# Kernel tuning notes

Measured on AMD Instinct MI355X. Metric: run time of the kernel, lower is better.

The kernel has to match this reference:

```python
import jax, jax.numpy as jnp
import numpy as np

WINDOW_SIZE = 11
SIGMA = 1.5
C1 = 0.01 ** 2
C2 = 0.03 ** 2


def _gaussian_window(window_size=WINDOW_SIZE, sigma=SIGMA):
    coords = jnp.arange(window_size, dtype=jnp.float32) - window_size // 2
    g = jnp.exp(-(coords ** 2) / (2.0 * sigma ** 2))
    g = g / g.sum()
    w3d = g[:, None, None] * g[None, :, None] * g[None, None, :]
    w3d = w3d / w3d.sum()
    return w3d[None, None]  # [1, 1, K, K, K] (OIDHW)


def _gconv3d(x, window):
    # depthwise 3D conv, SAME padding (pad = K//2), groups = C
    C = x.shape[1]
    w = jnp.broadcast_to(window, (C, 1) + window.shape[2:])
    pad = window.shape[-1] // 2
    return jax.lax.conv_general_dilated(
        x, w,
        window_strides=(1, 1, 1),
        padding=[(pad, pad)] * 3,
        dimension_numbers=("NCDHW", "OIDHW", "NCDHW"),
        feature_group_count=C,
    )


def setup_inputs() -> dict:
    key = jax.random.key(0)
    k1, k2 = jax.random.split(key)
    shape = (4, 1, 64, 192, 192)  # [B, C, D, H, W]
    pred = jax.random.uniform(k1, shape, dtype=jnp.float32)
    target = jax.random.uniform(k2, shape, dtype=jnp.float32)
    return {"pred": pred, "target": target}


def reference(pred, target):
    window = _gaussian_window()
    mu_p = _gconv3d(pred, window)
    mu_t = _gconv3d(target, window)
    mu_p_sq = mu_p ** 2
    mu_t_sq = mu_t ** 2
    mu_pt = mu_p * mu_t
    sigma_p_sq = _gconv3d(pred ** 2, window) - mu_p_sq
    sigma_t_sq = _gconv3d(target ** 2, window) - mu_t_sq
    sigma_pt = _gconv3d(pred * target, window) - mu_pt
    ssim_map = ((2.0 * mu_pt + C1) * (2.0 * sigma_pt + C2)) / (
        (mu_p_sq + mu_t_sq + C1) * (sigma_p_sq + sigma_t_sq + C2)
    )
    return 1.0 - ssim_map.mean()
```

## Files before the change

kernel.cpp:

```cpp
#include <hip/hip_runtime.h>


#define D_DIM 64
#define H_DIM 192
#define W_DIM 192
#define SLICE (H_DIM * W_DIM)
#define VOL   (D_DIM * SLICE)
#define NB    4
#define KS    11
#define RAD   5
#define TH    32
#define TW    48
#define HT    (TH + 2 * RAD)
#define WTT   (TW + 2 * RAD)
#define SPITCH 59
#define IP2   48
#define IPF2  (HT * IP2)
#define C1F   (0.01f * 0.01f)
#define C2F   (0.03f * 0.03f)

typedef _Float16 h4 __attribute__((ext_vector_type(4)));

__device__ __forceinline__ void make_window(float* g) {
    float s = 0.f;
#pragma unroll
    for (int i = 0; i < KS; ++i) {
        float c = (float)(i - RAD);
        g[i] = expf(-(c * c) * (1.0f / 4.5f));
        s += g[i];
    }
    float inv = 1.0f / s;
#pragma unroll
    for (int i = 0; i < KS; ++i) g[i] *= inv;
}

__global__ __launch_bounds__(256) void hw_blur_kernel(
    const float* __restrict__ pred, const float* __restrict__ targ,
    uint2* __restrict__ Xg, unsigned short* __restrict__ Yg, int b0) {
    __shared__ union U {
        float stage[2 * HT * SPITCH];
        unsigned short obuf[5 * TH * TW];
    } u;
    __shared__ _Float16 interm2[5 * IPF2];
    float* sp = u.stage;
    float* st = u.stage + HT * SPITCH;

    float g[KS];
    make_window(g);

    const int tid = threadIdx.x;
    const int d    = blockIdx.y;
    const int tile = blockIdx.x;
    const int h0 = (tile >> 2) * TH;
    const int w0 = (tile & 3) * TW;
    const int bl = blockIdx.z;

    const int in_base = (b0 + bl) * VOL + d * SLICE;

    for (int i = tid; i < HT * SPITCH; i += 256) {
        int y = i / SPITCH, x = i - y * SPITCH;
        int gh = h0 + y - RAD, gw = w0 + x - RAD;
        float pv = 0.f, tv = 0.f;
        if (x < WTT && (unsigned)gh < (unsigned)H_DIM && (unsigned)gw < (unsigned)W_DIM) {
            int idx = in_base + gh * W_DIM + gw;
            pv = pred[idx];
            tv = targ[idx];
        }
        sp[i] = pv;
        st[i] = tv;
    }
    __syncthreads();

    if (tid < 252) {
        const int y = tid / 6;
        const int x0 = (tid % 6) * 8;
        float wp[18], wt[18];
#pragma unroll
        for (int k = 0; k < 18; ++k) {
            wp[k] = sp[y * SPITCH + x0 + k];
            wt[k] = st[y * SPITCH + x0 + k];
        }
#pragma unroll
        for (int o = 0; o < 8; ++o) {
            float s0 = 0.f, s1 = 0.f, s2 = 0.f, s3 = 0.f, s4 = 0.f;
#pragma unroll
            for (int k = 0; k < KS; ++k) {
                float pv = wp[o + k], tv = wt[o + k], gk = g[k];
                s0 += gk * pv;
                s1 += gk * tv;
                s2 += gk * pv * pv;
                s3 += gk * tv * tv;
                s4 += gk * pv * tv;
            }
            int idx = y * IP2 + x0 + o;
            interm2[0 * IPF2 + idx] = (_Float16)s0;
            interm2[1 * IPF2 + idx] = (_Float16)s1;
            interm2[2 * IPF2 + idx] = (_Float16)s2;
            interm2[3 * IPF2 + idx] = (_Float16)s3;
            interm2[4 * IPF2 + idx] = (_Float16)s4;
        }
    }
    __syncthreads();

    if (tid < 240) {
        const int f = tid / TW;
        const int x = tid % TW;
        const _Float16* col = interm2 + f * IPF2 + x;
        unsigned short* ob = u.obuf + f * (TH * TW) + x;
        float acc[KS];
#pragma unroll
        for (int s = 0; s < KS; ++s) acc[s] = 0.f;
#pragma unroll
        for (int yy = 0; yy < HT; ++yy) {
            float v = (float)col[yy * IP2];
#pragma unroll
            for (int m = 0; m < KS; ++m) {
                if (yy < 10 && m < 10 - yy) continue;
                acc[(yy + m + 1) % KS] += g[10 - m] * v;
            }
            if (yy >= 10) {
                const int y = yy - 10;
                const int s = (yy + 1) % KS;
                _Float16 h = (_Float16)acc[s];
                ob[y * TW] = *(unsigned short*)&h;
                acc[s] = 0.f;
            }
        }
    }
    __syncthreads();

    const size_t pl_base = (size_t)(bl * D_DIM + d) * SLICE;
#pragma unroll
    for (int it = 0; it < 6; ++it) {
        int px = it * 256 + tid;
        int y = px / TW, x = px - y * TW;
        unsigned a0 = u.obuf[0 * (TH * TW) + px];
        unsigned a1 = u.obuf[1 * (TH * TW) + px];
        unsigned a2 = u.obuf[2 * (TH * TW) + px];
        unsigned a3 = u.obuf[3 * (TH * TW) + px];
        unsigned a4 = u.obuf[4 * (TH * TW) + px];
        size_t gi = pl_base + (size_t)(h0 + y) * W_DIM + (w0 + x);
        Xg[gi] = make_uint2(a0 | (a1 << 16), a2 | (a3 << 16));
        Yg[gi] = (unsigned short)a4;
    }
}


#define LOADP(s, q) do {                                                  \
    const int _o = (q) * SLICE;                                           \
    h4 _v = x4[_o];                                                       \
    w0[s] = (float)_v[0]; w1[s] = (float)_v[1];                           \
    w2[s] = (float)_v[2]; w3[s] = (float)_v[3];                           \
    w4[s] = (float)y1[_o];                                                \
} while (0)

#define SSIM_ACC(MP, MT, E2, T2, PT) do {                                 \
    float _mps = (MP) * (MP), _mts = (MT) * (MT), _mpt = (MP) * (MT);     \
    float _num = (2.f * _mpt + C1F) * (2.f * ((PT) - _mpt) + C2F);        \
    float _den = (_mps + _mts + C1F) *                                    \
                 (((E2) - _mps) + ((T2) - _mts) + C2F);                   \
    ssim_sum += _num * __builtin_amdgcn_rcpf(_den);                       \
} while (0)

#define EMIT_W(r, JHI) do {                                               \
    float _mp = 0.f, _mt = 0.f, _e2 = 0.f, _t2 = 0.f, _pt = 0.f;          \
    _Pragma("unroll")                                                     \
    for (int _j = 0; _j <= (JHI); ++_j) {                                 \
        const int _s = (1 + (r) + _j) % 11; const float _g = g[_j];       \
        _mp += _g * w0[_s]; _mt += _g * w1[_s]; _e2 += _g * w2[_s];       \
        _t2 += _g * w3[_s]; _pt += _g * w4[_s];                           \
    }                                                                     \
    SSIM_ACC(_mp, _mt, _e2, _t2, _pt);                                    \
} while (0)

#define EMIT_IN(d) do {                                                   \
    float _mp = 0.f, _mt = 0.f, _e2 = 0.f, _t2 = 0.f, _pt = 0.f;          \
    _Pragma("unroll")                                                     \
    for (int _j = 5 - (d); _j < 11; ++_j) {                               \
        const int _s = (d) - 5 + _j; const float _g = g[_j];              \
        _mp += _g * w0[_s]; _mt += _g * w1[_s]; _e2 += _g * w2[_s];       \
        _t2 += _g * w3[_s]; _pt += _g * w4[_s];                           \
    }                                                                     \
    SSIM_ACC(_mp, _mt, _e2, _t2, _pt);                                    \
} while (0)

#define STEP(r, q) do { LOADP(r, q); EMIT_W(r, 10); } while (0)

__global__ __launch_bounds__(256) void dblur_ssim_kernel(
    const h4* __restrict__ Xg, const _Float16* __restrict__ Yg,
    float* __restrict__ partials) {
    float g[KS];
    make_window(g);

    const int tid = threadIdx.x;
    const int bl = blockIdx.x / 144;
    const int hw = (blockIdx.x % 144) * 256 + tid;
    const int cb = bl * VOL + hw;
    const h4* x4 = Xg + cb;
    const _Float16* y1 = Yg + cb;

    float w0[KS], w1[KS], w2[KS], w3[KS], w4[KS];
    float ssim_sum = 0.f;

    if (blockIdx.y == 0) {
        LOADP(0, 0); LOADP(1, 1); LOADP(2, 2); LOADP(3, 3); LOADP(4, 4);
        LOADP(5, 5); LOADP(6, 6); LOADP(7, 7); LOADP(8, 8); LOADP(9, 9);
        LOADP(10, 10);
        EMIT_IN(0); EMIT_IN(1); EMIT_IN(2); EMIT_IN(3); EMIT_IN(4); EMIT_IN(5);
#pragma unroll 1
        for (int b = 0; b < 2; ++b) {
            const int qb = 11 + 11 * b;
            STEP(0, qb + 0); STEP(1, qb + 1); STEP(2, qb + 2); STEP(3, qb + 3);
            STEP(4, qb + 4); STEP(5, qb + 5); STEP(6, qb + 6); STEP(7, qb + 7);
            STEP(8, qb + 8); STEP(9, qb + 9); STEP(10, qb + 10);
        }
        STEP(0, 33); STEP(1, 34); STEP(2, 35); STEP(3, 36);
    } else {
        LOADP(5, 27); LOADP(6, 28); LOADP(7, 29); LOADP(8, 30); LOADP(9, 31);
        LOADP(10, 32); LOADP(0, 33); LOADP(1, 34); LOADP(2, 35); LOADP(3, 36);
        LOADP(4, 37);
        EMIT_W(4, 10);
        STEP(5, 38); STEP(6, 39); STEP(7, 40); STEP(8, 41); STEP(9, 42);
        STEP(10, 43);
        {
            const int qb = 44;
            STEP(0, qb + 0); STEP(1, qb + 1); STEP(2, qb + 2); STEP(3, qb + 3);
            STEP(4, qb + 4); STEP(5, qb + 5); STEP(6, qb + 6); STEP(7, qb + 7);
            STEP(8, qb + 8); STEP(9, qb + 9); STEP(10, qb + 10);
        }
        STEP(0, 55); STEP(1, 56); STEP(2, 57); STEP(3, 58); STEP(4, 59);
        STEP(5, 60); STEP(6, 61); STEP(7, 62); STEP(8, 63);
        EMIT_W(9, 9); EMIT_W(10, 8); EMIT_W(11, 7); EMIT_W(12, 6); EMIT_W(13, 5);
    }

    float a = ssim_sum;
#pragma unroll
    for (int off = 32; off > 0; off >>= 1) a += __shfl_down(a, off, 64);
    __shared__ float red[4];
    int lane = tid & 63, wv = tid >> 6;
    if (lane == 0) red[wv] = a;
    __syncthreads();
    if (tid == 0)
        partials[blockIdx.y * gridDim.x + blockIdx.x] =
            red[0] + red[1] + red[2] + red[3];
}

__global__ __launch_bounds__(256) void finalize_kernel(
    const float* __restrict__ partials, int n, float* __restrict__ out) {
    double a = 0.0;
    for (int i = threadIdx.x; i < n; i += 256) a += (double)partials[i];
#pragma unroll
    for (int off = 32; off > 0; off >>= 1) a += __shfl_down(a, off, 64);
    __shared__ double red[4];
    int lane = threadIdx.x & 63, wv = threadIdx.x >> 6;
    if (lane == 0) red[wv] = a;
    __syncthreads();
    if (threadIdx.x == 0) {
        double s = red[0] + red[1] + red[2] + red[3];
        out[0] = (float)(1.0 - s / (double)((long long)NB * VOL));
    }
}

extern "C" void kernel_launch(void* const* d_in, const int* in_sizes, int n_in,
                              void* d_out, int out_size, void* d_ws, size_t ws_size,
                              hipStream_t stream) {
    const float* pred = (const float*)d_in[0];
    const float* targ = (const float*)d_in[1];
    float* out = (float*)d_out;

    int G = 4;
    while (G > 1 && (size_t)G * VOL * 10 + 8192 > ws_size) G >>= 1;

    uint2* Xg = (uint2*)d_ws;
    unsigned short* Yg = (unsigned short*)((char*)d_ws + (size_t)G * VOL * 8);
    float* partials = (float*)((char*)d_ws + (size_t)G * VOL * 10);
    const int bpc = G * 144;
    const int nchunks = NB / G;

    for (int c = 0; c < nchunks; ++c) {
        hw_blur_kernel<<<dim3(24, D_DIM, G), 256, 0, stream>>>(
            pred, targ, Xg, Yg, c * G);
        dblur_ssim_kernel<<<dim3(bpc, 2), 256, 0, stream>>>(
            (const h4*)Xg, (const _Float16*)Yg, partials + c * 2 * bpc);
    }
    finalize_kernel<<<1, 256, 0, stream>>>(partials, NB * 288, out);
}
```

Baseline: 216.5 us.

## Process two pixels per thread with packed half2 shared and wider global accesses

The HW blur kernel now stores intermediates as packed half2 words, so each vertical-pass thread handles two adjacent columns over half the rows, and the output is written as 16-byte X and 4-byte Y vectors. The depth-blur SSIM kernel now has each thread process two horizontally adjacent pixels using 16-byte and 4-byte loads, which halves the number of blocks. The aim is fewer, wider memory transactions and fewer LDS accesses, at the cost of doubled register arrays (ten 11-element windows), which may lower occupancy or cause spills.

```diff
diff --git a/kernel.cpp b/kernel.cpp
--- a/kernel.cpp
+++ b/kernel.cpp
@@ -14,12 +14,13 @@
 #define HT    (TH + 2 * RAD)
 #define WTT   (TW + 2 * RAD)
 #define SPITCH 59
-#define IP2   48
-#define IPF2  (HT * IP2)
+#define IP32  25
+#define IPF32 (HT * IP32)
 #define C1F   (0.01f * 0.01f)
 #define C2F   (0.03f * 0.03f)
 
-typedef _Float16 h4 __attribute__((ext_vector_type(4)));
+typedef _Float16 h2v __attribute__((ext_vector_type(2)));
+typedef _Float16 h8v __attribute__((ext_vector_type(8)));
 
 __device__ __forceinline__ void make_window(float* g) {
     float s = 0.f;
@@ -32,6 +33,12 @@
     float inv = 1.0f / s;
 #pragma unroll
     for (int i = 0; i < KS; ++i) g[i] *= inv;
+}
+
+__device__ __forceinline__ unsigned pk(float a, float b) {
+    unsigned lo = __builtin_bit_cast(unsigned short, (_Float16)a);
+    unsigned hi = __builtin_bit_cast(unsigned short, (_Float16)b);
+    return lo | (hi << 16);
 }
 
 __global__ __launch_bounds__(256) void hw_blur_kernel(
@@ -39,9 +46,9 @@
     uint2* __restrict__ Xg, unsigned short* __restrict__ Yg, int b0) {
     __shared__ union U {
         float stage[2 * HT * SPITCH];
-        unsigned short obuf[5 * TH * TW];
+        unsigned obuf32[5 * TH * (TW / 2)];
     } u;
-    __shared__ _Float16 interm2[5 * IPF2];
+    __shared__ unsigned interm32[5 * IPF32];
     float* sp = u.stage;
     float* st = u.stage + HT * SPITCH;
 
@@ -80,50 +87,59 @@
             wp[k] = sp[y * SPITCH + x0 + k];
             wt[k] = st[y * SPITCH + x0 + k];
         }
-#pragma unroll
-        for (int o = 0; o < 8; ++o) {
-            float s0 = 0.f, s1 = 0.f, s2 = 0.f, s3 = 0.f, s4 = 0.f;
-#pragma unroll
-            for (int k = 0; k < KS; ++k) {
-                float pv = wp[o + k], tv = wt[o + k], gk = g[k];
-                s0 += gk * pv;
-                s1 += gk * tv;
-                s2 += gk * pv * pv;
-                s3 += gk * tv * tv;
-                s4 += gk * pv * tv;
+        const int ib = y * IP32 + (x0 >> 1);
+#pragma unroll
+        for (int o = 0; o < 8; o += 2) {
+            float r0[2], r1[2], r2[2], r3[2], r4[2];
+#pragma unroll
+            for (int c = 0; c < 2; ++c) {
+                float s0 = 0.f, s1 = 0.f, s2 = 0.f, s3 = 0.f, s4 = 0.f;
+#pragma unroll
+                for (int k = 0; k < KS; ++k) {
+                    float pv = wp[o + c + k], tv = wt[o + c + k], gk = g[k];
+                    s0 += gk * pv;
+                    s1 += gk * tv;
+                    s2 += gk * pv * pv;
+                    s3 += gk * tv * tv;
+                    s4 += gk * pv * tv;
+                }
+                r0[c] = s0; r1[c] = s1; r2[c] = s2; r3[c] = s3; r4[c] = s4;
             }
-            int idx = y * IP2 + x0 + o;
-            interm2[0 * IPF2 + idx] = (_Float16)s0;
-            interm2[1 * IPF2 + idx] = (_Float16)s1;
-            interm2[2 * IPF2 + idx] = (_Float16)s2;
-            interm2[3 * IPF2 + idx] = (_Float16)s3;
-            interm2[4 * IPF2 + idx] = (_Float16)s4;
+            int idx = ib + (o >> 1);
+            interm32[0 * IPF32 + idx] = pk(r0[0], r0[1]);
+            interm32[1 * IPF32 + idx] = pk(r1[0], r1[1]);
+            interm32[2 * IPF32 + idx] = pk(r2[0], r2[1]);
+            interm32[3 * IPF32 + idx] = pk(r3[0], r3[1]);
+            interm32[4 * IPF32 + idx] = pk(r4[0], r4[1]);
         }
     }
     __syncthreads();
 
     if (tid < 240) {
-        const int f = tid / TW;
-        const int x = tid % TW;
-        const _Float16* col = interm2 + f * IPF2 + x;
-        unsigned short* ob = u.obuf + f * (TH * TW) + x;
-        float acc[KS];
-#pragma unroll
-        for (int s = 0; s < KS; ++s) acc[s] = 0.f;
-#pragma unroll
-        for (int yy = 0; yy < HT; ++yy) {
-            float v = (float)col[yy * IP2];
+        const int f  = tid / 48;
+        const int r  = tid % 48;
+        const int hh = r / 24;
+        const int p  = r % 24;
+        const unsigned* col = interm32 + f * IPF32 + (hh * 16) * IP32 + p;
+        unsigned* ob = u.obuf32 + f * (TH * (TW / 2)) + (hh * 16) * (TW / 2) + p;
+        float acc0[KS], acc1[KS];
+#pragma unroll
+        for (int s = 0; s < KS; ++s) { acc0[s] = 0.f; acc1[s] = 0.f; }
+#pragma unroll
+        for (int yy = 0; yy < 26; ++yy) {
+            h2v hv = __builtin_bit_cast(h2v, col[yy * IP32]);
+            float v0 = (float)hv[0], v1 = (float)hv[1];
 #pragma unroll
             for (int m = 0; m < KS; ++m) {
                 if (yy < 10 && m < 10 - yy) continue;
-                acc[(yy + m + 1) % KS] += g[10 - m] * v;
+                const int s = (yy + m + 1) % KS;
+                acc0[s] += g[10 - m] * v0;
+                acc1[s] += g[10 - m] * v1;
             }
             if (yy >= 10) {
-                const int y = yy - 10;
                 const int s = (yy + 1) % KS;
-                _Float16 h = (_Float16)acc[s];
-                ob[y * TW] = *(unsigned short*)&h;
-                acc[s] = 0.f;
+                ob[(yy - 10) * (TW / 2)] = pk(acc0[s], acc1[s]);
+                acc0[s] = 0.f; acc1[s] = 0.f;
             }
         }
     }
@@ -131,27 +147,33 @@
 
     const size_t pl_base = (size_t)(bl * D_DIM + d) * SLICE;
 #pragma unroll
-    for (int it = 0; it < 6; ++it) {
-        int px = it * 256 + tid;
-        int y = px / TW, x = px - y * TW;
-        unsigned a0 = u.obuf[0 * (TH * TW) + px];
-        unsigned a1 = u.obuf[1 * (TH * TW) + px];
-        unsigned a2 = u.obuf[2 * (TH * TW) + px];
-        unsigned a3 = u.obuf[3 * (TH * TW) + px];
-        unsigned a4 = u.obuf[4 * (TH * TW) + px];
-        size_t gi = pl_base + (size_t)(h0 + y) * W_DIM + (w0 + x);
-        Xg[gi] = make_uint2(a0 | (a1 << 16), a2 | (a3 << 16));
-        Yg[gi] = (unsigned short)a4;
+    for (int it = 0; it < 3; ++it) {
+        int pr = it * 256 + tid;
+        int y = pr / 24, xp = pr % 24;
+        unsigned a0 = u.obuf32[0 * 768 + pr];
+        unsigned a1 = u.obuf32[1 * 768 + pr];
+        unsigned a2 = u.obuf32[2 * 768 + pr];
+        unsigned a3 = u.obuf32[3 * 768 + pr];
+        unsigned a4 = u.obuf32[4 * 768 + pr];
+        size_t gi = pl_base + (size_t)(h0 + y) * W_DIM + (w0 + 2 * xp);
+        uint4 xv = make_uint4((a0 & 0xffffu) | (a1 << 16),
+                              (a2 & 0xffffu) | (a3 << 16),
+                              (a0 >> 16) | (a1 & 0xffff0000u),
+                              (a2 >> 16) | (a3 & 0xffff0000u));
+        *(uint4*)(Xg + gi) = xv;
+        *(unsigned*)(Yg + gi) = a4;
     }
 }
 
 
 #define LOADP(s, q) do {                                                  \
-    const int _o = (q) * SLICE;                                           \
-    h4 _v = x4[_o];                                                       \
-    w0[s] = (float)_v[0]; w1[s] = (float)_v[1];                           \
-    w2[s] = (float)_v[2]; w3[s] = (float)_v[3];                           \
-    w4[s] = (float)y1[_o];                                                \
+    h8v _v = x8[(q) * (SLICE / 2)];                                       \
+    h2v _y = __builtin_bit_cast(h2v, y2[(q) * (SLICE / 2)]);              \
+    wa0[s] = (float)_v[0]; wa1[s] = (float)_v[1];                         \
+    wa2[s] = (float)_v[2]; wa3[s] = (float)_v[3];                         \
+    wb0[s] = (float)_v[4]; wb1[s] = (float)_v[5];                         \
+    wb2[s] = (float)_v[6]; wb3[s] = (float)_v[7];                         \
+    wa4[s] = (float)_y[0]; wb4[s] = (float)_y[1];                         \
 } while (0)
 
 #define SSIM_ACC(MP, MT, E2, T2, PT) do {                                 \
@@ -163,43 +185,52 @@
 } while (0)
 
 #define EMIT_W(r, JHI) do {                                               \
-    float _mp = 0.f, _mt = 0.f, _e2 = 0.f, _t2 = 0.f, _pt = 0.f;          \
+    float _ap = 0.f, _at = 0.f, _a2 = 0.f, _a3 = 0.f, _a4 = 0.f;          \
+    float _bp = 0.f, _bt = 0.f, _b2 = 0.f, _b3 = 0.f, _b4 = 0.f;          \
     _Pragma("unroll")                                                     \
     for (int _j = 0; _j <= (JHI); ++_j) {                                 \
         const int _s = (1 + (r) + _j) % 11; const float _g = g[_j];       \
-        _mp += _g * w0[_s]; _mt += _g * w1[_s]; _e2 += _g * w2[_s];       \
-        _t2 += _g * w3[_s]; _pt += _g * w4[_s];                           \
+        _ap += _g * wa0[_s]; _at += _g * wa1[_s]; _a2 += _g * wa2[_s];    \
+        _a3 += _g * wa3[_s]; _a4 += _g * wa4[_s];                         \
+        _bp += _g * wb0[_s]; _bt += _g * wb1[_s]; _b2 += _g * wb2[_s];    \
+        _b3 += _g * wb3[_s]; _b4 += _g * wb4[_s];                         \
     }                                                                     \
-    SSIM_ACC(_mp, _mt, _e2, _t2, _pt);                                    \
+    SSIM_ACC(_ap, _at, _a2, _a3, _a4);                                    \
+    SSIM_ACC(_bp, _bt, _b2, _b3, _b4);                                    \
 } while (0)
 
 #define EMIT_IN(d) do {                                                   \
-    float _mp = 0.f, _mt = 0.f, _e2 = 0.f, _t2 = 0.f, _pt = 0.f;          \
+    float _ap = 0.f, _at = 0.f, _a2 = 0.f, _a3 = 0.f, _a4 = 0.f;          \
+    float _bp = 0.f, _bt = 0.f, _b2 = 0.f, _b3 = 0.f, _b4 = 0.f;          \
     _Pragma("unroll")                                                     \
     for (int _j = 5 - (d); _j < 11; ++_j) {                               \
         const int _s = (d) - 5 + _j; const float _g = g[_j];              \
-        _mp += _g * w0[_s]; _mt += _g * w1[_s]; _e2 += _g * w2[_s];       \
-        _t2 += _g * w3[_s]; _pt += _g * w4[_s];                           \
+        _ap += _g * wa0[_s]; _at += _g * wa1[_s]; _a2 += _g * wa2[_s];    \
+        _a3 += _g * wa3[_s]; _a4 += _g * wa4[_s];                         \
+        _bp += _g * wb0[_s]; _bt += _g * wb1[_s]; _b2 += _g * wb2[_s];    \
+        _b3 += _g * wb3[_s]; _b4 += _g * wb4[_s];                         \
     }                                                                     \
-    SSIM_ACC(_mp, _mt, _e2, _t2, _pt);                                    \
+    SSIM_ACC(_ap, _at, _a2, _a3, _a4);                                    \
+    SSIM_ACC(_bp, _bt, _b2, _b3, _b4);                                    \
 } while (0)
 
 #define STEP(r, q) do { LOADP(r, q); EMIT_W(r, 10); } while (0)
 
 __global__ __launch_bounds__(256) void dblur_ssim_kernel(
-    const h4* __restrict__ Xg, const _Float16* __restrict__ Yg,
+    const uint2* __restrict__ Xg, const unsigned short* __restrict__ Yg,
     float* __restrict__ partials) {
     float g[KS];
     make_window(g);
 
     const int tid = threadIdx.x;
-    const int bl = blockIdx.x / 144;
-    const int hw = (blockIdx.x % 144) * 256 + tid;
-    const int cb = bl * VOL + hw;
-    const h4* x4 = Xg + cb;
-    const _Float16* y1 = Yg + cb;
-
-    float w0[KS], w1[KS], w2[KS], w3[KS], w4[KS];
+    const int bl = blockIdx.x / 72;
+    const int hw0 = (blockIdx.x % 72) * 512 + tid * 2;
+    const int cb = bl * VOL + hw0;
+    const h8v* x8 = (const h8v*)Xg + (cb >> 1);
+    const unsigned* y2 = (const unsigned*)Yg + (cb >> 1);
+
+    float wa0[KS], wa1[KS], wa2[KS], wa3[KS], wa4[KS];
+    float wb0[KS], wb1[KS], wb2[KS], wb3[KS], wb4[KS];
     float ssim_sum = 0.f;
 
     if (blockIdx.y == 0) {
@@ -222,7 +253,8 @@
         EMIT_W(4, 10);
         STEP(5, 38); STEP(6, 39); STEP(7, 40); STEP(8, 41); STEP(9, 42);
         STEP(10, 43);
-        {
+#pragma unroll 1
+        for (int b = 0; b < 1; ++b) {
             const int qb = 44;
             STEP(0, qb + 0); STEP(1, qb + 1); STEP(2, qb + 2); STEP(3, qb + 3);
             STEP(4, qb + 4); STEP(5, qb + 5); STEP(6, qb + 6); STEP(7, qb + 7);
@@ -274,14 +306,14 @@
     uint2* Xg = (uint2*)d_ws;
     unsigned short* Yg = (unsigned short*)((char*)d_ws + (size_t)G * VOL * 8);
     float* partials = (float*)((char*)d_ws + (size_t)G * VOL * 10);
-    const int bpc = G * 144;
+    const int bpc = G * 72;
     const int nchunks = NB / G;
 
     for (int c = 0; c < nchunks; ++c) {
         hw_blur_kernel<<<dim3(24, D_DIM, G), 256, 0, stream>>>(
             pred, targ, Xg, Yg, c * G);
         dblur_ssim_kernel<<<dim3(bpc, 2), 256, 0, stream>>>(
-            (const h4*)Xg, (const _Float16*)Yg, partials + c * 2 * bpc);
-    }
-    finalize_kernel<<<1, 256, 0, stream>>>(partials, NB * 288, out);
-}
+            Xg, Yg, partials + c * 2 * bpc);
+    }
+    finalize_kernel<<<1, 256, 0, stream>>>(partials, NB * 144, out);
+}
```

Result: slower. 223.6 us (+3.3%).
